# Optimization experiments

Measured on AMD Instinct MI355X. Metric: run time of the kernel, lower is better.

## Reference

```python
import jax, jax.numpy as jnp
import numpy as np

LAM = 0.1   # smooth_param
EPS = 1e-8  # torch cosine_similarity eps


def setup_inputs() -> dict:
    key = jax.random.key(0)
    k1, k2, k3 = jax.random.split(key, 3)
    B, num_supp, num_query, T, D = 8, 5, 128, 16, 2048
    supp = jax.random.normal(k1, (B, num_supp, T, D), jnp.float32)
    query = jax.random.normal(k2, (B, num_query, T, D), jnp.float32)
    query_ys = jax.random.randint(k3, (B * num_query,), 0, num_supp)
    return {"supp": supp, "query": query, "query_ys": query_ys}


def _cosine_dist(supp, query):
    # supp: (B, ns, T, D), query: (B, nq, T, D)
    # dist[b,q,s,l,m] = 1 - cos(supp[b,s,l], query[b,q,m]); batch order (b,q,s)
    B, ns, T, D = supp.shape
    nq = query.shape[1]
    dots = jnp.einsum('bsld,bqmd->bqslm', supp, query)
    sn = jnp.linalg.norm(supp, axis=-1)   # (B, ns, T)
    qn = jnp.linalg.norm(query, axis=-1)  # (B, nq, T)
    denom = jnp.maximum(sn[:, None, :, :, None] * qn[:, :, None, None, :], EPS)
    dist = 1.0 - dots / denom
    return dist.reshape(B * nq * ns, T, T)


def _dtw(dist):
    # Relaxed (soft-min) OTAM band DP. dist: (N, T, T) -> (N,)
    # opt grid is (T, T+2) with zero-padded columns m=0 and m=T+1.
    N, T, _ = dist.shape
    dist_pad = jnp.pad(dist, ((0, 0), (0, 0), (1, 1)))  # (N, T, T+2)
    # Row l=0: opt[0,m] = cumsum of dist_pad[0, :m+1]
    row0 = jnp.cumsum(dist_pad[:, 0, :], axis=-1)  # (N, T+2)

    m_idx = jnp.arange(1, T + 2)
    boundary = (m_idx == 1) | (m_idx == T + 1)  # 3-way softmin only at band edges

    def row_step(prev_row, dist_row):
        # prev_row: (N, T+2) = opt[l-1]; dist_row: (N, T+2) = dist_pad[:, l]
        def col_step(left, xs):
            diag, up, d, is_b = xs  # each (N,) except is_b scalar bool
            s2 = jnp.logaddexp(-diag / LAM, -left / LAM)        # {diag, left}
            s3 = jnp.logaddexp(s2, -up / LAM)                   # + {up}
            val = -LAM * jnp.where(is_b, s3, s2) + d
            return val, val

        xs = (prev_row[:, :-1].T, prev_row[:, 1:].T, dist_row[:, 1:].T, boundary)
        init = jnp.zeros((N,), dist_row.dtype)  # opt[l, 0] = 0
        _, cols = jax.lax.scan(col_step, init, xs)  # (T+1, N)
        new_row = jnp.concatenate([init[:, None], cols.T], axis=1)  # (N, T+2)
        return new_row, None

    rows = jnp.swapaxes(dist_pad[:, 1:, :], 0, 1)  # (T-1, N, T+2)
    final_row, _ = jax.lax.scan(row_step, row0, rows)
    return final_row[:, -1]  # opt[:, T-1, T+1]


def _cross_entropy(logits, labels):
    logp = jax.nn.log_softmax(logits, axis=-1)
    return -jnp.mean(jnp.take_along_axis(logp, labels[:, None], axis=1))


def reference(supp, query, query_ys):
    ns = supp.shape[1]
    dist = _cosine_dist(supp, query)            # (B*nq*ns, T, T)
    tam1 = _dtw(dist).reshape(-1, ns)           # forward-direction alignment
    tam2 = _dtw(dist[:, ::-1, ::-1]).reshape(-1, ns)  # flipped (dims 1,2)
    loss1 = _cross_entropy(-tam1, query_ys)
    loss2 = _cross_entropy(-tam2, query_ys)
    loss = 0.5 * (loss1 + loss2)
    tam = 0.5 * (tam1 + tam2)
    return loss, tam
```

## Files before the change

kernel.cpp:

```cpp
#include <hip/hip_runtime.h>
#include <hip/hip_bf16.h>

#define NB   8
#define NS   5
#define NQ   128
#define TT   16
#define DD   2048
#define NROW 1024
#define NSROW (NB * NS * TT)
#define LDB  2056
#define LAMI 10.0f
#define LAMF 0.1f

typedef __attribute__((ext_vector_type(8))) short  short8;
typedef __attribute__((ext_vector_type(4))) float  float4v;

static __device__ __forceinline__ unsigned int f2bf2(float x, float y) {
    union { float f; unsigned int u; } a, b; a.f = x; b.f = y;
    unsigned int ra = a.u + 0x7fffu + ((a.u >> 16) & 1u);
    unsigned int rb = b.u + 0x7fffu + ((b.u >> 16) & 1u);
    return (ra >> 16) | (rb & 0xffff0000u);
}

static __device__ __forceinline__ float lse2f(float x, float y) {
    float mx = fmaxf(x, y), mn = fminf(x, y);
    return mx + __logf(1.0f + __expf(mn - mx));
}

__global__ __launch_bounds__(256) void
preproc_supp(const float* __restrict__ supp, unsigned short* __restrict__ suppBf,
             float* __restrict__ suppSq)
{
    const int wave = threadIdx.x >> 6, lane = threadIdx.x & 63;
    const int row = blockIdx.x * 4 + wave;
    const float* src = supp + (size_t)row * DD;
    unsigned short* dst = suppBf + (size_t)row * DD;
    float ss = 0.f;
    #pragma unroll
    for (int i = 0; i < 8; ++i) {
        float4 v = *reinterpret_cast<const float4*>(src + i * 256 + lane * 4);
        uint2 pv = { f2bf2(v.x, v.y), f2bf2(v.z, v.w) };
        *reinterpret_cast<uint2*>(dst + i * 256 + lane * 4) = pv;
        ss += v.x * v.x + v.y * v.y + v.z * v.z + v.w * v.w;
    }
    #pragma unroll
    for (int off = 32; off >= 1; off >>= 1) ss += __shfl_xor(ss, off, 64);
    if (lane == 0) suppSq[row] = ss;
}

__global__ __launch_bounds__(512, 4) void
dist_dtw_kernel(const unsigned short* __restrict__ suppBf, const float* __restrict__ suppSq,
                const float* __restrict__ query,
                float* __restrict__ out_tam, float* __restrict__ t1w, float* __restrict__ t2w)
{
    __shared__ __align__(16) unsigned short sB[TT * LDB];
    __shared__ float ssq[96];
    __shared__ float distS[NS][TT][TT];
    __shared__ float tamv[16];

    const int tid  = threadIdx.x;
    const int blk  = blockIdx.x;
    const int wave = tid >> 6;
    const int lane = tid & 63;
    const int fr   = lane & 15;
    const int quad = lane >> 4;

    {
        const int r = tid >> 5;
        const int c = tid & 31;
        const float* src = query + (size_t)(blk * TT + r) * DD;
        float ss = 0.f;
        #pragma unroll
        for (int i = 0; i < 16; ++i) {
            float4 v = *reinterpret_cast<const float4*>(src + (c + i * 32) * 4);
            uint2 pv = { f2bf2(v.x, v.y), f2bf2(v.z, v.w) };
            *reinterpret_cast<uint2*>(&sB[r * LDB + (c + i * 32) * 4]) = pv;
            ss += v.x * v.x + v.y * v.y + v.z * v.z + v.w * v.w;
        }
        #pragma unroll
        for (int off = 16; off >= 1; off >>= 1) ss += __shfl_xor(ss, off, 32);
        if ((tid & 31) == 0) ssq[80 + r] = ss;
        if (tid < 80) ssq[tid] = suppSq[(blk >> 7) * (NS * TT) + tid];
    }
    __syncthreads();

    float4v acc0 = {0.f, 0.f, 0.f, 0.f}, acc1 = {0.f, 0.f, 0.f, 0.f};
    if (wave < NS) {
        const unsigned short* ap =
            suppBf + ((size_t)((blk >> 7) * NS + wave) * TT + fr) * DD + quad * 8;
        const unsigned short* bp = &sB[fr * LDB + quad * 8];
        #pragma unroll 8
        for (int k = 0; k < 64; k += 2) {
            short8 a0 = *reinterpret_cast<const short8*>(ap + k * 32);
            short8 a1 = *reinterpret_cast<const short8*>(ap + k * 32 + 32);
            short8 b0 = *reinterpret_cast<const short8*>(bp + k * 32);
            short8 b1 = *reinterpret_cast<const short8*>(bp + k * 32 + 32);
            acc0 = __builtin_amdgcn_mfma_f32_16x16x32_bf16(a0, b0, acc0, 0, 0, 0);
            acc1 = __builtin_amdgcn_mfma_f32_16x16x32_bf16(a1, b1, acc1, 0, 0, 0);
        }
        float qn = sqrtf(ssq[80 + fr]);
        #pragma unroll
        for (int r = 0; r < 4; ++r) {
            int l = quad * 4 + r;
            float denom = fmaxf(sqrtf(ssq[wave * 16 + l]) * qn, 1e-8f);
            distS[wave][l][fr] = 1.0f - (acc0[r] + acc1[r]) / denom;
        }
    }
    __syncthreads();

    if (wave < NS && (lane & 31) <= 17) {
        const int g   = lane & 31;
        const int dir = lane >> 5;
        const int s   = wave;
        float val = 0.f, vprev = 0.f;
        #pragma unroll
        for (int t = 1; t <= 32; ++t) {
            float left = __shfl_up(val,   1, 32);
            float diag = __shfl_up(vprev, 1, 32);
            int l = t - g;
            if (g >= 1 && l >= 0 && l <= 15) {
                float d = 0.f;
                if (g <= 16) d = dir ? distS[s][15 - l][16 - g] : distS[s][l][g - 1];
                float nv;
                if (l == 0) {
                    nv = left + d;
                } else if (g == 1 || g == 17) {
                    nv = -LAMF * lse2f(lse2f(-diag * LAMI, -left * LAMI), -val * LAMI) + d;
                } else {
                    float lo2 = fminf(diag, left), hi2 = fmaxf(diag, left);
                    nv = lo2 - LAMF * __logf(1.0f + __expf((lo2 - hi2) * LAMI)) + d;
                }
                vprev = val; val = nv;
            }
        }
        if (g == 17) tamv[s * 2 + dir] = val;
    }
    __syncthreads();

    if (tid < NS) {
        float t1 = tamv[2 * tid], t2 = tamv[2 * tid + 1];
        int n = blk * NS + tid;
        t1w[n] = t1;
        t2w[n] = t2;
        out_tam[n] = 0.5f * (t1 + t2);
    }
}

__global__ __launch_bounds__(1024) void
loss_kernel(const float* __restrict__ t1w, const float* __restrict__ t2w,
            const int* __restrict__ ys, float* __restrict__ out)
{
    __shared__ float red[16];
    const int row = threadIdx.x;

    float t1[NS], t2[NS];
    #pragma unroll
    for (int s = 0; s < NS; ++s) { t1[s] = t1w[row * NS + s]; t2[s] = t2w[row * NS + s]; }
    const int y = ys[row];

    float mx1 = -t1[0], mx2 = -t2[0];
    #pragma unroll
    for (int s = 1; s < NS; ++s) { mx1 = fmaxf(mx1, -t1[s]); mx2 = fmaxf(mx2, -t2[s]); }
    float s1 = 0.f, s2 = 0.f;
    #pragma unroll
    for (int s = 0; s < NS; ++s) { s1 += __expf(-t1[s] - mx1); s2 += __expf(-t2[s] - mx2); }
    float lse1  = mx1 + __logf(s1);
    float lse2v = mx2 + __logf(s2);

    float ty1 = t1[0], ty2 = t2[0];
    #pragma unroll
    for (int s = 1; s < NS; ++s) { if (y == s) { ty1 = t1[s]; ty2 = t2[s]; } }

    float c = 0.5f * ((lse1 + ty1) + (lse2v + ty2));

    #pragma unroll
    for (int off = 32; off >= 1; off >>= 1) c += __shfl_down(c, off, 64);
    if ((row & 63) == 0) red[row >> 6] = c;
    __syncthreads();
    if (row == 0) {
        float tot = 0.f;
        #pragma unroll
        for (int i = 0; i < 16; ++i) tot += red[i];
        out[0] = tot * (1.0f / (float)NROW);
    }
}

extern "C" void kernel_launch(void* const* d_in, const int* in_sizes, int n_in,
                              void* d_out, int out_size, void* d_ws, size_t ws_size,
                              hipStream_t stream) {
    const float* supp  = (const float*)d_in[0];
    const float* query = (const float*)d_in[1];
    const int*   ys    = (const int*)d_in[2];
    float* out = (float*)d_out;

    float* t1w    = (float*)d_ws;
    float* t2w    = t1w + NROW * NS;
    float* suppSq = t2w + NROW * NS;
    unsigned short* suppBf = (unsigned short*)(suppSq + NSROW);

    preproc_supp<<<NSROW / 4, 256, 0, stream>>>(supp, suppBf, suppSq);
    dist_dtw_kernel<<<NROW, 512, 0, stream>>>(suppBf, suppSq, query, out + 1, t1w, t2w);
    loss_kernel<<<1, 1024, 0, stream>>>(t1w, t2w, ys, out);
}
```

Before: 252.5 us.

## Stream query directly into MFMA registers, drop LDS staging, shrink block to 5 waves

```diff
diff --git a/kernel.cpp b/kernel.cpp
--- a/kernel.cpp
+++ b/kernel.cpp
@@ -8,7 +8,7 @@
 #define DD   2048
 #define NROW 1024
 #define NSROW (NB * NS * TT)
-#define LDB  2056
+#define PF   4
 #define LAMI 10.0f
 #define LAMF 0.1f
 
@@ -48,12 +48,11 @@
     if (lane == 0) suppSq[row] = ss;
 }
 
-__global__ __launch_bounds__(512, 4) void
+__global__ __launch_bounds__(320, 5) void
 dist_dtw_kernel(const unsigned short* __restrict__ suppBf, const float* __restrict__ suppSq,
                 const float* __restrict__ query,
                 float* __restrict__ out_tam, float* __restrict__ t1w, float* __restrict__ t2w)
 {
-    __shared__ __align__(16) unsigned short sB[TT * LDB];
     __shared__ float ssq[96];
     __shared__ float distS[NS][TT][TT];
     __shared__ float tamv[16];
@@ -65,50 +64,63 @@
     const int fr   = lane & 15;
     const int quad = lane >> 4;
 
+    if (tid < 80) ssq[tid] = suppSq[(blk >> 7) * (NS * TT) + tid];
+
+    const unsigned short* ap =
+        suppBf + ((size_t)((blk >> 7) * NS + wave) * TT + fr) * DD + quad * 8;
+    const float* qp = query + ((size_t)(blk * TT + fr)) * DD + quad * 8;
+
+    float4 qbuf[PF][2];
+    short8 abuf[PF];
+    #pragma unroll
+    for (int i = 0; i < PF; ++i) {
+        qbuf[i][0] = *reinterpret_cast<const float4*>(qp + i * 32);
+        qbuf[i][1] = *reinterpret_cast<const float4*>(qp + i * 32 + 4);
+        abuf[i]    = *reinterpret_cast<const short8*>(ap + i * 32);
+    }
+
+    float4v acc = {0.f, 0.f, 0.f, 0.f};
+    float qss = 0.f;
+
+    #pragma unroll
+    for (int k = 0; k < 64; ++k) {
+        const int sl = k % PF;
+        float4 v0 = qbuf[sl][0], v1 = qbuf[sl][1];
+        short8 a  = abuf[sl];
+        if (k + PF < 64) {
+            qbuf[sl][0] = *reinterpret_cast<const float4*>(qp + (k + PF) * 32);
+            qbuf[sl][1] = *reinterpret_cast<const float4*>(qp + (k + PF) * 32 + 4);
+            abuf[sl]    = *reinterpret_cast<const short8*>(ap + (k + PF) * 32);
+        }
+        union { short8 s8; unsigned int u[4]; } bu;
+        bu.u[0] = f2bf2(v0.x, v0.y);
+        bu.u[1] = f2bf2(v0.z, v0.w);
+        bu.u[2] = f2bf2(v1.x, v1.y);
+        bu.u[3] = f2bf2(v1.z, v1.w);
+        qss += v0.x * v0.x + v0.y * v0.y + v0.z * v0.z + v0.w * v0.w
+             + v1.x * v1.x + v1.y * v1.y + v1.z * v1.z + v1.w * v1.w;
+        acc = __builtin_amdgcn_mfma_f32_16x16x32_bf16(a, bu.s8, acc, 0, 0, 0);
+        if ((k & 15) == 15 && k < 63)
+            __builtin_amdgcn_s_barrier();
+    }
+
+    qss += __shfl_xor(qss, 16, 64);
+    qss += __shfl_xor(qss, 32, 64);
+    if (wave == 0 && lane < 16) ssq[80 + lane] = qss;
+    __syncthreads();
+
     {
-        const int r = tid >> 5;
-        const int c = tid & 31;
-        const float* src = query + (size_t)(blk * TT + r) * DD;
-        float ss = 0.f;
-        #pragma unroll
-        for (int i = 0; i < 16; ++i) {
-            float4 v = *reinterpret_cast<const float4*>(src + (c + i * 32) * 4);
-            uint2 pv = { f2bf2(v.x, v.y), f2bf2(v.z, v.w) };
-            *reinterpret_cast<uint2*>(&sB[r * LDB + (c + i * 32) * 4]) = pv;
-            ss += v.x * v.x + v.y * v.y + v.z * v.z + v.w * v.w;
-        }
-        #pragma unroll
-        for (int off = 16; off >= 1; off >>= 1) ss += __shfl_xor(ss, off, 32);
-        if ((tid & 31) == 0) ssq[80 + r] = ss;
-        if (tid < 80) ssq[tid] = suppSq[(blk >> 7) * (NS * TT) + tid];
-    }
-    __syncthreads();
-
-    float4v acc0 = {0.f, 0.f, 0.f, 0.f}, acc1 = {0.f, 0.f, 0.f, 0.f};
-    if (wave < NS) {
-        const unsigned short* ap =
-            suppBf + ((size_t)((blk >> 7) * NS + wave) * TT + fr) * DD + quad * 8;
-        const unsigned short* bp = &sB[fr * LDB + quad * 8];
-        #pragma unroll 8
-        for (int k = 0; k < 64; k += 2) {
-            short8 a0 = *reinterpret_cast<const short8*>(ap + k * 32);
-            short8 a1 = *reinterpret_cast<const short8*>(ap + k * 32 + 32);
-            short8 b0 = *reinterpret_cast<const short8*>(bp + k * 32);
-            short8 b1 = *reinterpret_cast<const short8*>(bp + k * 32 + 32);
-            acc0 = __builtin_amdgcn_mfma_f32_16x16x32_bf16(a0, b0, acc0, 0, 0, 0);
-            acc1 = __builtin_amdgcn_mfma_f32_16x16x32_bf16(a1, b1, acc1, 0, 0, 0);
-        }
         float qn = sqrtf(ssq[80 + fr]);
         #pragma unroll
         for (int r = 0; r < 4; ++r) {
             int l = quad * 4 + r;
             float denom = fmaxf(sqrtf(ssq[wave * 16 + l]) * qn, 1e-8f);
-            distS[wave][l][fr] = 1.0f - (acc0[r] + acc1[r]) / denom;
+            distS[wave][l][fr] = 1.0f - acc[r] / denom;
         }
     }
     __syncthreads();
 
-    if (wave < NS && (lane & 31) <= 17) {
+    if ((lane & 31) <= 17) {
         const int g   = lane & 31;
         const int dir = lane >> 5;
         const int s   = wave;
@@ -199,6 +211,6 @@
     unsigned short* suppBf = (unsigned short*)(suppSq + NSROW);
 
     preproc_supp<<<NSROW / 4, 256, 0, stream>>>(supp, suppBf, suppSq);
-    dist_dtw_kernel<<<NROW, 512, 0, stream>>>(suppBf, suppSq, query, out + 1, t1w, t2w);
+    dist_dtw_kernel<<<NROW, 320, 0, stream>>>(suppBf, suppSq, query, out + 1, t1w, t2w);
     loss_kernel<<<1, 1024, 0, stream>>>(t1w, t2w, ys, out);
 }
```

Result: slower. 980.9 us (+288.4%).
